# Kernel tuning notes

Hardware: AMD Instinct MI355X
Metric: run time of the kernel (lower is better)

Reference implementation:

```python
import jax, jax.numpy as jnp
import numpy as np

N_NODES, N_EDGES, DIM, N_GRAPHS = 200000, 400000, 256, 2048


def _mlp_params(key, dim):
    # MLP([dim, dim//2, dim//4, 1]) -> 3 Linear layers
    k1, k2, k3 = jax.random.split(key, 3)
    def lin(k, fi, fo):
        s = 1.0 / np.sqrt(fi)
        kw, kb = jax.random.split(k)
        W = jax.random.uniform(kw, (fi, fo), jnp.float32, -s, s)
        b = jax.random.uniform(kb, (fo,), jnp.float32, -s, s)
        return W, b
    W1, b1 = lin(k1, dim, dim // 2)
    W2, b2 = lin(k2, dim // 2, dim // 4)
    W3, b3 = lin(k3, dim // 4, 1)
    return W1, b1, W2, b2, W3, b3


def setup_inputs() -> dict:
    key = jax.random.key(0)
    kn, ke, kin, kie, kpn, kpe = jax.random.split(key, 6)
    emb_nodes = jax.random.normal(kn, (N_NODES, DIM), jnp.float32)
    emb_edges = jax.random.normal(ke, (N_EDGES, DIM), jnp.float32)
    node_index = jnp.sort(jax.random.randint(kin, (N_NODES,), 0, N_GRAPHS, jnp.int32))
    edge_index = jnp.sort(jax.random.randint(kie, (N_EDGES,), 0, N_GRAPHS, jnp.int32))
    Wn1, bn1, Wn2, bn2, Wn3, bn3 = _mlp_params(kpn, DIM)
    We1, be1, We2, be2, We3, be3 = _mlp_params(kpe, DIM)
    return {
        "emb_nodes": emb_nodes, "emb_edges": emb_edges,
        "node_index": node_index, "edge_index": edge_index,
        "Wn1": Wn1, "bn1": bn1, "Wn2": Wn2, "bn2": bn2, "Wn3": Wn3, "bn3": bn3,
        "We1": We1, "be1": be1, "We2": We2, "be2": be2, "We3": We3, "be3": be3,
        "num_graphs": N_GRAPHS,
    }


def _gated_att_pool(src, index, W1, b1, W2, b2, W3, b3, num_segments):
    # att MLP: dim -> dim/2 -> dim/4 -> 1 (ReLU between hidden layers)
    h = jax.nn.relu(src @ W1 + b1)
    h = jax.nn.relu(h @ W2 + b2)
    logits = (h @ W3 + b3).reshape(-1)  # [N]
    # scatter_softmax over segments (numerically stable)
    m = jax.ops.segment_max(logits, index, num_segments=num_segments)
    e = jnp.exp(logits - m[index])
    s = jax.ops.segment_sum(e, index, num_segments=num_segments)
    att = (e / s[index])[:, None]  # [N,1]
    # weighted scatter_add -> [num_segments, dim]
    return jax.ops.segment_sum(att * src, index, num_segments=num_segments)


def reference(emb_nodes, emb_edges, node_index, edge_index,
              Wn1, bn1, Wn2, bn2, Wn3, bn3,
              We1, be1, We2, be2, We3, be3, num_graphs):
    nodes_pooled = _gated_att_pool(emb_nodes, node_index, Wn1, bn1, Wn2, bn2, Wn3, bn3, num_graphs)
    edges_pooled = _gated_att_pool(emb_edges, edge_index, We1, be1, We2, be2, We3, be3, num_graphs)
    return nodes_pooled, edges_pooled
```

## Files before the change

kernel.cpp:

```cpp
#include <hip/hip_runtime.h>

typedef unsigned short ushort_t;
typedef __attribute__((ext_vector_type(8))) short short8;
typedef __attribute__((ext_vector_type(4))) short short4v;
typedef __attribute__((ext_vector_type(4))) float f32x4;

__device__ __forceinline__ ushort_t f2bf(float f) {
    union { float f; unsigned int u; } c; c.f = f;
    unsigned int r = c.u + 0x7fffu + ((c.u >> 16) & 1u);
    return (ushort_t)(r >> 16);
}

__global__ __launch_bounds__(256) void build_wfrags(
    const float* __restrict__ W1, const float* __restrict__ W2,
    ushort_t* __restrict__ W1f, ushort_t* __restrict__ W2f)
{
    int tid = blockIdx.x * 256 + threadIdx.x;
    if (tid < 32768) {
        int j = tid & 7, l = (tid >> 3) & 63, fi = tid >> 9;
        int nt = fi >> 3, kt = fi & 7;
        int n = nt * 16 + (l & 15);
        int k = kt * 32 + (l >> 4) * 8 + j;
        W1f[tid] = f2bf(W1[k * 128 + n]);
    } else if (tid < 40960) {
        int u = tid - 32768;
        int j = u & 7, l = (u >> 3) & 63, fi = u >> 9;
        int nt = fi >> 2, kt = fi & 3;
        int n = nt * 16 + (l & 15);
        int k = kt * 32 + (l >> 4) * 8 + j;
        W2f[u] = f2bf(W2[k * 64 + n]);
    }
}

#define TPB 4

__global__ __launch_bounds__(256) void mlp_logits(
    const float* __restrict__ X, const ushort_t* __restrict__ W1f,
    const ushort_t* __restrict__ W2f, const float* __restrict__ b1,
    const float* __restrict__ b2, const float* __restrict__ W3,
    const float* __restrict__ b3, float* __restrict__ logits)
{
    __shared__ ushort_t xs[16 * 264];
    __shared__ ushort_t h1s[16 * 136];
    __shared__ float part[4][16];

    const int t = threadIdx.x;
    const int w = t >> 6, lane = t & 63;
    const int q = lane >> 4, c16 = lane & 15;

    short8 w1f[2][8];
    for (int i = 0; i < 2; ++i) {
        int nt = 2 * w + i;
        for (int kt = 0; kt < 8; ++kt)
            w1f[i][kt] = ((const short8*)W1f)[(nt * 8 + kt) * 64 + lane];
    }
    short8 w2f[4];
    for (int kt = 0; kt < 4; ++kt)
        w2f[kt] = ((const short8*)W2f)[(w * 4 + kt) * 64 + lane];
    float bias1[2];
    bias1[0] = b1[(2 * w) * 16 + c16];
    bias1[1] = b1[(2 * w + 1) * 16 + c16];
    const float bias2 = b2[w * 16 + c16];
    const float w3v = W3[w * 16 + c16];
    const float b3v = b3[0];

    const int rowb0 = blockIdx.x * (16 * TPB);

    for (int sub = 0; sub < TPB; ++sub) {
        const int rowb = rowb0 + sub * 16;

        for (int i = 0; i < 4; ++i) {
            int r = i * 4 + w;
            const f32x4 v = *(const f32x4*)(X + (size_t)(rowb + r) * 256 + lane * 4);
            short4v h;
            h[0] = (short)f2bf(v[0]); h[1] = (short)f2bf(v[1]);
            h[2] = (short)f2bf(v[2]); h[3] = (short)f2bf(v[3]);
            *(short4v*)(xs + r * 264 + lane * 4) = h;
        }
        __syncthreads();

        f32x4 acc0 = {0.f, 0.f, 0.f, 0.f}, acc1 = {0.f, 0.f, 0.f, 0.f};
        for (int kt = 0; kt < 8; ++kt) {
            short8 a = *(const short8*)(xs + c16 * 264 + kt * 32 + q * 8);
            acc0 = __builtin_amdgcn_mfma_f32_16x16x32_bf16(a, w1f[0][kt], acc0, 0, 0, 0);
            acc1 = __builtin_amdgcn_mfma_f32_16x16x32_bf16(a, w1f[1][kt], acc1, 0, 0, 0);
        }
        for (int i = 0; i < 2; ++i) {
            f32x4 a = i ? acc1 : acc0;
            int col = (2 * w + i) * 16 + c16;
            for (int reg = 0; reg < 4; ++reg) {
                float v = fmaxf(a[reg] + bias1[i], 0.f);
                h1s[(q * 4 + reg) * 136 + col] = f2bf(v);
            }
        }
        __syncthreads();

        f32x4 acc2 = {0.f, 0.f, 0.f, 0.f};
        for (int kt = 0; kt < 4; ++kt) {
            short8 a = *(const short8*)(h1s + c16 * 136 + kt * 32 + q * 8);
            acc2 = __builtin_amdgcn_mfma_f32_16x16x32_bf16(a, w2f[kt], acc2, 0, 0, 0);
        }
        float p[4];
        for (int reg = 0; reg < 4; ++reg)
            p[reg] = fmaxf(acc2[reg] + bias2, 0.f) * w3v;
        for (int m = 1; m < 16; m <<= 1)
            for (int reg = 0; reg < 4; ++reg)
                p[reg] += __shfl_xor(p[reg], m);
        if (c16 == 0)
            for (int reg = 0; reg < 4; ++reg)
                part[w][q * 4 + reg] = p[reg];
        __syncthreads();
        if (t < 16)
            logits[rowb + t] = part[0][t] + part[1][t] + part[2][t] + part[3][t] + b3v;
    }
}

__global__ __launch_bounds__(256) void pool(
    const float* __restrict__ X, const int* __restrict__ idx,
    const float* __restrict__ logits, float* __restrict__ out, int nrows)
{
    const int g = blockIdx.x;
    const int t = threadIdx.x;
    const int w = t >> 6, lane = t & 63;

    int lo = 0, hi = nrows;
    while (lo < hi) { int mid = (lo + hi) >> 1; if (idx[mid] < g) lo = mid + 1; else hi = mid; }
    const int start = lo;
    hi = nrows;
    while (lo < hi) { int mid = (lo + hi) >> 1; if (idx[mid] < g + 1) lo = mid + 1; else hi = mid; }
    const int cnt = lo - start;

    __shared__ float red[4];
    __shared__ float att[256];

    float m = -3.0e38f;
    for (int i = t; i < cnt; i += 256) m = fmaxf(m, logits[start + i]);
    for (int o = 32; o; o >>= 1) m = fmaxf(m, __shfl_down(m, o));
    if (lane == 0) red[w] = m;
    __syncthreads();
    m = fmaxf(fmaxf(red[0], red[1]), fmaxf(red[2], red[3]));
    __syncthreads();

    float s = 0.f;
    for (int i = t; i < cnt; i += 256) s += __expf(logits[start + i] - m);
    for (int o = 32; o; o >>= 1) s += __shfl_down(s, o);
    if (lane == 0) red[w] = s;
    __syncthreads();
    s = red[0] + red[1] + red[2] + red[3];
    const float inv = (cnt > 0) ? 1.f / s : 0.f;

    float acc = 0.f;
    for (int base = 0; base < cnt; base += 256) {
        const int c = min(256, cnt - base);
        __syncthreads();
        if (t < c) att[t] = __expf(logits[start + base + t] - m) * inv;
        __syncthreads();
        const float* xp = X + (size_t)(start + base) * 256 + t;
        int r = 0;
        for (; r + 4 <= c; r += 4) {
            float a0 = att[r], a1 = att[r + 1], a2 = att[r + 2], a3 = att[r + 3];
            acc += a0 * xp[(size_t)(r + 0) * 256] + a1 * xp[(size_t)(r + 1) * 256]
                 + a2 * xp[(size_t)(r + 2) * 256] + a3 * xp[(size_t)(r + 3) * 256];
        }
        for (; r < c; ++r) acc += att[r] * xp[(size_t)r * 256];
    }
    out[(size_t)g * 256 + t] = acc;
}


extern "C" void kernel_launch(void* const* d_in, const int* in_sizes, int n_in,
                              void* d_out, int out_size, void* d_ws, size_t ws_size,
                              hipStream_t stream) {
    const float* Xn  = (const float*)d_in[0];
    const float* Xe  = (const float*)d_in[1];
    const int* idxn  = (const int*)d_in[2];
    const int* idxe  = (const int*)d_in[3];
    const float* Wn1 = (const float*)d_in[4];
    const float* bn1 = (const float*)d_in[5];
    const float* Wn2 = (const float*)d_in[6];
    const float* bn2 = (const float*)d_in[7];
    const float* Wn3 = (const float*)d_in[8];
    const float* bn3 = (const float*)d_in[9];
    const float* We1 = (const float*)d_in[10];
    const float* be1 = (const float*)d_in[11];
    const float* We2 = (const float*)d_in[12];
    const float* be2 = (const float*)d_in[13];
    const float* We3 = (const float*)d_in[14];
    const float* be3 = (const float*)d_in[15];
    float* out = (float*)d_out;

    char* ws = (char*)d_ws;
    ushort_t* W1f_n = (ushort_t*)(ws + 0);
    ushort_t* W2f_n = (ushort_t*)(ws + 65536);
    ushort_t* W1f_e = (ushort_t*)(ws + 81920);
    ushort_t* W2f_e = (ushort_t*)(ws + 147456);
    float* log_n = (float*)(ws + 163840);
    float* log_e = (float*)(ws + 963840);

    build_wfrags<<<160, 256, 0, stream>>>(Wn1, Wn2, W1f_n, W2f_n);
    build_wfrags<<<160, 256, 0, stream>>>(We1, We2, W1f_e, W2f_e);

    mlp_logits<<<200000 / (16 * TPB), 256, 0, stream>>>(Xn, W1f_n, W2f_n, bn1, bn2, Wn3, bn3, log_n);
    mlp_logits<<<400000 / (16 * TPB), 256, 0, stream>>>(Xe, W1f_e, W2f_e, be1, be2, We3, be3, log_e);

    pool<<<2048, 256, 0, stream>>>(Xn, idxn, log_n, out, 200000);
    pool<<<2048, 256, 0, stream>>>(Xe, idxe, log_e, out + (size_t)2048 * 256, 400000);
}
```

Before: 845.1 us.

## Stage MLP weights in LDS, give each wave full row tiles, vectorize pooling

The MLP kernel now copies both bf16 weight fragment sets into 80KB of dynamic LDS and has each of 8 waves process whole 16-row tiles on its own: it loads X straight to registers, runs all 8 N-tiles of layer 1 and all 4 of layer 2, and writes logits with no block-wide barriers. The pool kernel splits rows across waves, uses float4 loads and computes attention weights inline, then reduces the four wave partials through LDS. The aim is to remove per-tile __syncthreads and redundant X staging and to widen pool loads. In exchange the large LDS footprint and 512-thread blocks limit occupancy, and every block re-copies the weights from global memory.

New measurement: 844.7 us. About the same (-0.0%).

```diff
diff --git a/kernel.cpp b/kernel.cpp
--- a/kernel.cpp
+++ b/kernel.cpp
@@ -2,7 +2,6 @@
 
 typedef unsigned short ushort_t;
 typedef __attribute__((ext_vector_type(8))) short short8;
-typedef __attribute__((ext_vector_type(4))) short short4v;
 typedef __attribute__((ext_vector_type(4))) float f32x4;
 
 __device__ __forceinline__ ushort_t f2bf(float f) {
@@ -32,86 +31,113 @@
     }
 }
 
-#define TPB 4
-
-__global__ __launch_bounds__(256) void mlp_logits(
+#define MLP_WAVES 8
+#define MLP_TPW 2
+#define MLP_LDS_BYTES (65536 + 16384 + MLP_WAVES * 16 * 136 * 2)
+
+__global__ __launch_bounds__(512) void mlp_logits(
     const float* __restrict__ X, const ushort_t* __restrict__ W1f,
     const ushort_t* __restrict__ W2f, const float* __restrict__ b1,
     const float* __restrict__ b2, const float* __restrict__ W3,
-    const float* __restrict__ b3, float* __restrict__ logits)
+    const float* __restrict__ b3, float* __restrict__ logits, int nsub)
 {
-    __shared__ ushort_t xs[16 * 264];
-    __shared__ ushort_t h1s[16 * 136];
-    __shared__ float part[4][16];
+    extern __shared__ __align__(16) char smem[];
+    ushort_t* W1s    = (ushort_t*)smem;
+    ushort_t* W2s    = (ushort_t*)(smem + 65536);
+    ushort_t* h1base = (ushort_t*)(smem + 81920);
 
     const int t = threadIdx.x;
     const int w = t >> 6, lane = t & 63;
     const int q = lane >> 4, c16 = lane & 15;
 
-    short8 w1f[2][8];
-    for (int i = 0; i < 2; ++i) {
-        int nt = 2 * w + i;
-        for (int kt = 0; kt < 8; ++kt)
-            w1f[i][kt] = ((const short8*)W1f)[(nt * 8 + kt) * 64 + lane];
-    }
-    short8 w2f[4];
-    for (int kt = 0; kt < 4; ++kt)
-        w2f[kt] = ((const short8*)W2f)[(w * 4 + kt) * 64 + lane];
-    float bias1[2];
-    bias1[0] = b1[(2 * w) * 16 + c16];
-    bias1[1] = b1[(2 * w + 1) * 16 + c16];
-    const float bias2 = b2[w * 16 + c16];
-    const float w3v = W3[w * 16 + c16];
+    {
+        const f32x4* s1 = (const f32x4*)W1f; f32x4* d1 = (f32x4*)W1s;
+        for (int i = t; i < 4096; i += 512) d1[i] = s1[i];
+        const f32x4* s2 = (const f32x4*)W2f; f32x4* d2 = (f32x4*)W2s;
+        for (int i = t; i < 1024; i += 512) d2[i] = s2[i];
+    }
+    __syncthreads();
+
+    float bias1[8], bias2[4], w3v[4];
+    #pragma unroll
+    for (int nt = 0; nt < 8; ++nt) bias1[nt] = b1[nt * 16 + c16];
+    #pragma unroll
+    for (int nt = 0; nt < 4; ++nt) bias2[nt] = b2[nt * 16 + c16];
+    #pragma unroll
+    for (int nt = 0; nt < 4; ++nt) w3v[nt] = W3[nt * 16 + c16];
     const float b3v = b3[0];
 
-    const int rowb0 = blockIdx.x * (16 * TPB);
-
-    for (int sub = 0; sub < TPB; ++sub) {
-        const int rowb = rowb0 + sub * 16;
-
-        for (int i = 0; i < 4; ++i) {
-            int r = i * 4 + w;
-            const f32x4 v = *(const f32x4*)(X + (size_t)(rowb + r) * 256 + lane * 4);
-            short4v h;
-            h[0] = (short)f2bf(v[0]); h[1] = (short)f2bf(v[1]);
-            h[2] = (short)f2bf(v[2]); h[3] = (short)f2bf(v[3]);
-            *(short4v*)(xs + r * 264 + lane * 4) = h;
-        }
-        __syncthreads();
-
-        f32x4 acc0 = {0.f, 0.f, 0.f, 0.f}, acc1 = {0.f, 0.f, 0.f, 0.f};
+    ushort_t* hw = h1base + w * (16 * 136);
+
+    for (int sub = 0; sub < MLP_TPW; ++sub) {
+        const int s = (blockIdx.x * MLP_WAVES + w) * MLP_TPW + sub;
+        if (s >= nsub) break;
+        const float* xp = X + (size_t)(s * 16 + c16) * 256 + q * 8;
+
+        f32x4 xv[16];
+        #pragma unroll
         for (int kt = 0; kt < 8; ++kt) {
-            short8 a = *(const short8*)(xs + c16 * 264 + kt * 32 + q * 8);
-            acc0 = __builtin_amdgcn_mfma_f32_16x16x32_bf16(a, w1f[0][kt], acc0, 0, 0, 0);
-            acc1 = __builtin_amdgcn_mfma_f32_16x16x32_bf16(a, w1f[1][kt], acc1, 0, 0, 0);
-        }
-        for (int i = 0; i < 2; ++i) {
-            f32x4 a = i ? acc1 : acc0;
-            int col = (2 * w + i) * 16 + c16;
-            for (int reg = 0; reg < 4; ++reg) {
-                float v = fmaxf(a[reg] + bias1[i], 0.f);
-                h1s[(q * 4 + reg) * 136 + col] = f2bf(v);
+            xv[2 * kt]     = *(const f32x4*)(xp + kt * 32);
+            xv[2 * kt + 1] = *(const f32x4*)(xp + kt * 32 + 4);
+        }
+
+        f32x4 acc[8];
+        #pragma unroll
+        for (int nt = 0; nt < 8; ++nt) acc[nt] = (f32x4){0.f, 0.f, 0.f, 0.f};
+        #pragma unroll
+        for (int kt = 0; kt < 8; ++kt) {
+            short8 a;
+            #pragma unroll
+            for (int j = 0; j < 4; ++j) {
+                a[j]     = (short)f2bf(xv[2 * kt][j]);
+                a[4 + j] = (short)f2bf(xv[2 * kt + 1][j]);
             }
-        }
-        __syncthreads();
-
-        f32x4 acc2 = {0.f, 0.f, 0.f, 0.f};
+            #pragma unroll
+            for (int nt = 0; nt < 8; ++nt) {
+                short8 bf = *(const short8*)(W1s + ((nt * 8 + kt) * 64 + lane) * 8);
+                acc[nt] = __builtin_amdgcn_mfma_f32_16x16x32_bf16(a, bf, acc[nt], 0, 0, 0);
+            }
+        }
+
+        #pragma unroll
+        for (int nt = 0; nt < 8; ++nt)
+            #pragma unroll
+            for (int reg = 0; reg < 4; ++reg)
+                hw[(q * 4 + reg) * 136 + nt * 16 + c16] =
+                    f2bf(fmaxf(acc[nt][reg] + bias1[nt], 0.f));
+
+        f32x4 acc2[4];
+        #pragma unroll
+        for (int nt = 0; nt < 4; ++nt) acc2[nt] = (f32x4){0.f, 0.f, 0.f, 0.f};
+        #pragma unroll
         for (int kt = 0; kt < 4; ++kt) {
-            short8 a = *(const short8*)(h1s + c16 * 136 + kt * 32 + q * 8);
-            acc2 = __builtin_amdgcn_mfma_f32_16x16x32_bf16(a, w2f[kt], acc2, 0, 0, 0);
-        }
+            short8 a = *(const short8*)(hw + c16 * 136 + kt * 32 + q * 8);
+            #pragma unroll
+            for (int nt = 0; nt < 4; ++nt) {
+                short8 bf = *(const short8*)(W2s + ((nt * 4 + kt) * 64 + lane) * 8);
+                acc2[nt] = __builtin_amdgcn_mfma_f32_16x16x32_bf16(a, bf, acc2[nt], 0, 0, 0);
+            }
+        }
+
         float p[4];
-        for (int reg = 0; reg < 4; ++reg)
-            p[reg] = fmaxf(acc2[reg] + bias2, 0.f) * w3v;
-        for (int m = 1; m < 16; m <<= 1)
+        #pragma unroll
+        for (int reg = 0; reg < 4; ++reg) {
+            float v = 0.f;
+            #pragma unroll
+            for (int nt = 0; nt < 4; ++nt)
+                v += fmaxf(acc2[nt][reg] + bias2[nt], 0.f) * w3v[nt];
+            p[reg] = v;
+        }
+        #pragma unroll
+        for (int msk = 1; msk < 16; msk <<= 1)
+            #pragma unroll
             for (int reg = 0; reg < 4; ++reg)
-                p[reg] += __shfl_xor(p[reg], m);
-        if (c16 == 0)
+                p[reg] += __shfl_xor(p[reg], msk);
+        if (c16 == 0) {
+            #pragma unroll
             for (int reg = 0; reg < 4; ++reg)
-                part[w][q * 4 + reg] = p[reg];
-        __syncthreads();
-        if (t < 16)
-            logits[rowb + t] = part[0][t] + part[1][t] + part[2][t] + part[3][t] + b3v;
+                logits[s * 16 + q * 4 + reg] = p[reg] + b3v;
+        }
     }
 }
 
@@ -130,41 +156,54 @@
     while (lo < hi) { int mid = (lo + hi) >> 1; if (idx[mid] < g + 1) lo = mid + 1; else hi = mid; }
     const int cnt = lo - start;
 
-    __shared__ float red[4];
-    __shared__ float att[256];
+    __shared__ float red[8];
+    __shared__ float parts[4][256];
+
+    const float* lg = logits + start;
 
     float m = -3.0e38f;
-    for (int i = t; i < cnt; i += 256) m = fmaxf(m, logits[start + i]);
-    for (int o = 32; o; o >>= 1) m = fmaxf(m, __shfl_down(m, o));
+    for (int i = t; i < cnt; i += 256) m = fmaxf(m, lg[i]);
+    #pragma unroll
+    for (int o = 32; o; o >>= 1) m = fmaxf(m, __shfl_xor(m, o));
     if (lane == 0) red[w] = m;
     __syncthreads();
     m = fmaxf(fmaxf(red[0], red[1]), fmaxf(red[2], red[3]));
-    __syncthreads();
-
-    float s = 0.f;
-    for (int i = t; i < cnt; i += 256) s += __expf(logits[start + i] - m);
-    for (int o = 32; o; o >>= 1) s += __shfl_down(s, o);
-    if (lane == 0) red[w] = s;
-    __syncthreads();
-    s = red[0] + red[1] + red[2] + red[3];
-    const float inv = (cnt > 0) ? 1.f / s : 0.f;
-
-    float acc = 0.f;
-    for (int base = 0; base < cnt; base += 256) {
-        const int c = min(256, cnt - base);
-        __syncthreads();
-        if (t < c) att[t] = __expf(logits[start + base + t] - m) * inv;
-        __syncthreads();
-        const float* xp = X + (size_t)(start + base) * 256 + t;
-        int r = 0;
-        for (; r + 4 <= c; r += 4) {
-            float a0 = att[r], a1 = att[r + 1], a2 = att[r + 2], a3 = att[r + 3];
-            acc += a0 * xp[(size_t)(r + 0) * 256] + a1 * xp[(size_t)(r + 1) * 256]
-                 + a2 * xp[(size_t)(r + 2) * 256] + a3 * xp[(size_t)(r + 3) * 256];
-        }
-        for (; r < c; ++r) acc += att[r] * xp[(size_t)r * 256];
-    }
-    out[(size_t)g * 256 + t] = acc;
+
+    float ssum = 0.f;
+    for (int i = t; i < cnt; i += 256) ssum += __expf(lg[i] - m);
+    #pragma unroll
+    for (int o = 32; o; o >>= 1) ssum += __shfl_xor(ssum, o);
+    if (lane == 0) red[4 + w] = ssum;
+    __syncthreads();
+    ssum = red[4] + red[5] + red[6] + red[7];
+    const float inv = (cnt > 0) ? 1.f / ssum : 0.f;
+
+    f32x4 acc = {0.f, 0.f, 0.f, 0.f};
+    const float* xb = X + (size_t)start * 256 + lane * 4;
+    int r = w;
+    for (; r + 12 < cnt; r += 16) {
+        float a0 = __expf(lg[r] - m);
+        float a1 = __expf(lg[r + 4] - m);
+        float a2 = __expf(lg[r + 8] - m);
+        float a3 = __expf(lg[r + 12] - m);
+        f32x4 x0 = *(const f32x4*)(xb + (size_t)(r) * 256);
+        f32x4 x1 = *(const f32x4*)(xb + (size_t)(r + 4) * 256);
+        f32x4 x2 = *(const f32x4*)(xb + (size_t)(r + 8) * 256);
+        f32x4 x3 = *(const f32x4*)(xb + (size_t)(r + 12) * 256);
+        acc += a0 * x0;
+        acc += a1 * x1;
+        acc += a2 * x2;
+        acc += a3 * x3;
+    }
+    for (; r < cnt; r += 4) {
+        float a = __expf(lg[r] - m);
+        f32x4 xv = *(const f32x4*)(xb + (size_t)r * 256);
+        acc += a * xv;
+    }
+    #pragma unroll
+    for (int j = 0; j < 4; ++j) parts[w][lane * 4 + j] = acc[j] * inv;
+    __syncthreads();
+    out[(size_t)g * 256 + t] = parts[0][t] + parts[1][t] + parts[2][t] + parts[3][t];
 }
 
 
@@ -197,12 +236,20 @@
     float* log_n = (float*)(ws + 163840);
     float* log_e = (float*)(ws + 963840);
 
+    (void)hipFuncSetAttribute((const void*)mlp_logits,
+                              hipFuncAttributeMaxDynamicSharedMemorySize,
+                              MLP_LDS_BYTES);
+
     build_wfrags<<<160, 256, 0, stream>>>(Wn1, Wn2, W1f_n, W2f_n);
     build_wfrags<<<160, 256, 0, stream>>>(We1, We2, W1f_e, W2f_e);
 
-    mlp_logits<<<200000 / (16 * TPB), 256, 0, stream>>>(Xn, W1f_n, W2f_n, bn1, bn2, Wn3, bn3, log_n);
-    mlp_logits<<<400000 / (16 * TPB), 256, 0, stream>>>(Xe, W1f_e, W2f_e, be1, be2, We3, be3, log_e);
-
+    const int nsub_n = 200000 / 16, nsub_e = 400000 / 16;
+    const int gpb = MLP_WAVES * MLP_TPW;
+    mlp_logits<<<(nsub_n + gpb - 1) / gpb, 512, MLP_LDS_BYTES, stream>>>(
+        Xn, W1f_n, W2f_n, bn1, bn2, Wn3, bn3, log_n, nsub_n);
     pool<<<2048, 256, 0, stream>>>(Xn, idxn, log_n, out, 200000);
+
+    mlp_logits<<<(nsub_e + gpb - 1) / gpb, 512, MLP_LDS_BYTES, stream>>>(
+        Xe, W1f_e, W2f_e, be1, be2, We3, be3, log_e, nsub_e);
     pool<<<2048, 256, 0, stream>>>(Xe, idxe, log_e, out + (size_t)2048 * 256, 400000);
 }
```
